# Performance work log

Measured on AMD Instinct MI355X. Metric: run time of the kernel, lower is better.

Reference implementation:

```python
import jax, jax.numpy as jnp
import numpy as np


def _laplacian_kernel(x, z, bandwidth):
    x_sq = jnp.sum(x * x, axis=-1, keepdims=True)          # [N, 1]
    z_sq = jnp.sum(z * z, axis=-1)[None, :]                # [1, M]
    d2 = x_sq + z_sq - 2.0 * jnp.einsum('nd,md->nm', x, z)  # [N, M]
    d = jnp.sqrt(jnp.maximum(d2, 0.0))
    return jnp.exp(-d / bandwidth)


def setup_inputs() -> dict:
    key = jax.random.key(0)
    k1, k2, k3 = jax.random.split(key, 3)
    N, M, D, Y = 8192, 20000, 1024, 256
    batch = jax.random.normal(k1, (N, D), dtype=jnp.float32)
    centers = jax.random.normal(k2, (M, D), dtype=jnp.float32)
    weight = jax.random.normal(k3, (M, Y), dtype=jnp.float32) * 0.02
    return {"batch": batch, "centers": centers, "weight": weight, "bandwidth": 10}


def reference(batch, centers, weight, bandwidth):
    kmat = _laplacian_kernel(batch, centers, float(bandwidth))  # [N, M]
    pred = kmat @ weight                                        # [N, Y]
    return pred
```

## Files before the change

kernel.cpp:

```cpp
#include <hip/hip_runtime.h>
#include <stdint.h>

#define N_ROWS 8192
#define D_DIM  1024
#define M_CENT 20000
#define M_PAD  20224
#define M_TILES 79
#define Y_DIM  256
#define BM 64
#define BN 256
#define MSPLIT 8
#define TILES_PER_SPLIT 10
#define LDSP_STRIDE 264
#define NKT 32
#define PANEL_X (NKT * 512)
#define NKT_M 632
#define PANEL_W (NKT_M * 512)


typedef __attribute__((ext_vector_type(4))) float  f32x4;
typedef __attribute__((ext_vector_type(8))) __bf16 bf16x8;

__device__ __forceinline__ unsigned short f2bf(float f) {
    union { float f; unsigned u; } v; v.f = f;
    unsigned u = v.u;
    u += 0x7FFFu + ((u >> 16) & 1u);
    return (unsigned short)(u >> 16);
}

__global__ void pack_rows_kernel(const float* __restrict__ src,
                                 unsigned short* __restrict__ dst,
                                 float* __restrict__ sq, int nrows_valid) {
    int row = blockIdx.x;
    int t = threadIdx.x;
    int p = row >> 4, m = row & 15;
    float s = 0.f;
    ushort4 o = make_ushort4(0, 0, 0, 0);
    if (row < nrows_valid) {
        float4 v = ((const float4*)(src + (size_t)row * D_DIM))[t];
        s = v.x * v.x + v.y * v.y + v.z * v.z + v.w * v.w;
        o.x = f2bf(v.x); o.y = f2bf(v.y); o.z = f2bf(v.z); o.w = f2bf(v.w);
    }
    size_t obase = (size_t)p * PANEL_X + (size_t)(t >> 3) * 512
                 + (size_t)((t >> 1) & 3) * 128 + m * 8 + (t & 1) * 4;
    *(ushort4*)(dst + obase) = o;
    __shared__ float red[4];
    for (int off = 32; off; off >>= 1) s += __shfl_down(s, off, 64);
    if ((t & 63) == 0) red[t >> 6] = s;
    __syncthreads();
    if (t == 0) sq[row] = red[0] + red[1] + red[2] + red[3];
}

__global__ void pack_wT_kernel(const float* __restrict__ w,
                               unsigned short* __restrict__ wTp) {
    __shared__ float tile[32][33];
    int m0 = blockIdx.x * 32;
    int y0 = blockIdx.y * 32;
    int tx = threadIdx.x & 31;
    int ty = threadIdx.x >> 5;
    #pragma unroll
    for (int i = 0; i < 4; ++i) {
        int mm = m0 + ty + i * 8;
        float v = (mm < M_CENT) ? w[(size_t)mm * Y_DIM + y0 + tx] : 0.f;
        tile[tx][ty + i * 8] = v;
    }
    __syncthreads();
    #pragma unroll
    for (int i = 0; i < 4; ++i) {
        int yl = ty + i * 8;
        int p = (y0 >> 4) + (yl >> 4);
        size_t off = (size_t)p * PANEL_W + (size_t)(m0 >> 5) * 512
                   + (size_t)(tx >> 3) * 128 + (yl & 15) * 8 + (tx & 7);
        wTp[off] = f2bf(tile[yl][tx]);
    }
}

__global__ void __launch_bounds__(256, 2)
fused_kernel(const unsigned short* __restrict__ Xp,
             const unsigned short* __restrict__ Zp,
             const unsigned short* __restrict__ WTp,
             const float* __restrict__ xsq,
             const float* __restrict__ zsq,
             const int* __restrict__ bwp,
             float* __restrict__ out) {
    __shared__ unsigned short lds_p[BM * LDSP_STRIDE];
    __shared__ float lds_xsq[BM];

    const int t    = threadIdx.x;
    const int wave = t >> 6;
    const int lane = t & 63;
    const int quad = lane >> 4;
    const int l16  = lane & 15;
    const int lane8 = lane * 8;

    const int row0 = blockIdx.x * BM;
    int mt = blockIdx.y * TILES_PER_SPLIT;
    int mt_end = mt + TILES_PER_SPLIT;
    if (mt_end > M_TILES) mt_end = M_TILES;

    int bwi = *bwp;
    float bw;
    if (bwi > 0 && bwi < 1000000) bw = (float)bwi;
    else { union { int i; float f; } u; u.i = bwi; bw = u.f; }
    const float inv_bw = 1.0f / bw;

    if (t < BM) lds_xsq[t] = xsq[row0 + t];

    const unsigned short* xp0 = Xp + (size_t)(row0 >> 4) * PANEL_X + lane8;

    const f32x4 vzero = {0.f, 0.f, 0.f, 0.f};
    f32x4 Oacc[16];
    #pragma unroll
    for (int i = 0; i < 16; ++i) Oacc[i] = vzero;

    #pragma unroll 1
    for (; mt < mt_end; ++mt) {
        const int m0 = mt * BN;
        const unsigned short* zp0 = Zp + (size_t)(mt * 16 + wave * 4) * PANEL_X + lane8;

        float zqv[4];
        #pragma unroll
        for (int jt = 0; jt < 4; ++jt)
            zqv[jt] = zsq[m0 + wave * 64 + jt * 16 + l16];

        f32x4 S[16];
        #pragma unroll
        for (int i = 0; i < 16; ++i) S[i] = vzero;

        bf16x8 ae[4], be[4], ao[4], bo[4];
        #pragma unroll
        for (int i = 0; i < 4; ++i) {
            ae[i] = *(const bf16x8*)(xp0 + (size_t)i * PANEL_X);
            be[i] = *(const bf16x8*)(zp0 + (size_t)i * PANEL_X);
        }
        #pragma unroll 1
        for (int kt2 = 0; kt2 < NKT / 2; ++kt2) {
            const unsigned short* xk = xp0 + (size_t)(2 * kt2 + 1) * 512;
            const unsigned short* zk = zp0 + (size_t)(2 * kt2 + 1) * 512;
            #pragma unroll
            for (int i = 0; i < 4; ++i) {
                ao[i] = *(const bf16x8*)(xk + (size_t)i * PANEL_X);
                bo[i] = *(const bf16x8*)(zk + (size_t)i * PANEL_X);
            }
            #pragma unroll
            for (int it = 0; it < 4; ++it)
                #pragma unroll
                for (int jt = 0; jt < 4; ++jt)
                    S[it * 4 + jt] = __builtin_amdgcn_mfma_f32_16x16x32_bf16(
                        ae[it], be[jt], S[it * 4 + jt], 0, 0, 0);
            #pragma unroll
            for (int i = 0; i < 4; ++i) {
                ae[i] = *(const bf16x8*)(xk + 512 + (size_t)i * PANEL_X);
                be[i] = *(const bf16x8*)(zk + 512 + (size_t)i * PANEL_X);
            }
            #pragma unroll
            for (int it = 0; it < 4; ++it)
                #pragma unroll
                for (int jt = 0; jt < 4; ++jt)
                    S[it * 4 + jt] = __builtin_amdgcn_mfma_f32_16x16x32_bf16(
                        ao[it], bo[jt], S[it * 4 + jt], 0, 0, 0);
        }

        __syncthreads();
        #pragma unroll
        for (int it = 0; it < 4; ++it) {
            #pragma unroll
            for (int jt = 0; jt < 4; ++jt) {
                f32x4 s4 = S[it * 4 + jt];
                const int col = wave * 64 + jt * 16 + l16;
                const float zq = zqv[jt];
                #pragma unroll
                for (int r = 0; r < 4; ++r) {
                    const int row = it * 16 + quad * 4 + r;
                    float d2 = lds_xsq[row] + zq - 2.0f * s4[r];
                    d2 = fmaxf(d2, 0.f);
                    float p = __expf(-sqrtf(d2) * inv_bw);
                    lds_p[row * LDSP_STRIDE + col] = f2bf(p);
                }
            }
        }
        __syncthreads();

        #pragma unroll
        for (int ks = 0; ks < 8; ++ks) {
            const int koff = ks * 32 + quad * 8;
            bf16x8 a[4], b[4];
            #pragma unroll
            for (int rt = 0; rt < 4; ++rt)
                a[rt] = *(const bf16x8*)&lds_p[(rt * 16 + l16) * LDSP_STRIDE + koff];
            #pragma unroll
            for (int ct = 0; ct < 4; ++ct)
                b[ct] = *(const bf16x8*)(WTp + (size_t)(wave * 4 + ct) * PANEL_W
                                             + (size_t)(mt * 8 + ks) * 512 + lane8);
            #pragma unroll
            for (int rt = 0; rt < 4; ++rt)
                #pragma unroll
                for (int ct = 0; ct < 4; ++ct)
                    Oacc[rt * 4 + ct] = __builtin_amdgcn_mfma_f32_16x16x32_bf16(
                        a[rt], b[ct], Oacc[rt * 4 + ct], 0, 0, 0);
        }
    }

    #pragma unroll
    for (int rt = 0; rt < 4; ++rt) {
        #pragma unroll
        for (int ct = 0; ct < 4; ++ct) {
            f32x4 v = Oacc[rt * 4 + ct];
            const int y = wave * 64 + ct * 16 + l16;
            #pragma unroll
            for (int r = 0; r < 4; ++r) {
                const int row = row0 + rt * 16 + quad * 4 + r;
                atomicAdd(&out[(size_t)row * Y_DIM + y], v[r]);
            }
        }
    }
}

extern "C" void kernel_launch(void* const* d_in, const int* in_sizes, int n_in,
                              void* d_out, int out_size, void* d_ws, size_t ws_size,
                              hipStream_t stream) {
    const float* X = (const float*)d_in[0];
    const float* Z = (const float*)d_in[1];
    const float* W = (const float*)d_in[2];
    const int*  bw = (const int*)d_in[3];
    float* out = (float*)d_out;

    char* ws = (char*)d_ws;
    size_t off = 0;
    unsigned short* Xp  = (unsigned short*)(ws + off); off += (size_t)N_ROWS * D_DIM * 2;
    unsigned short* Zp  = (unsigned short*)(ws + off); off += (size_t)M_PAD * D_DIM * 2;
    unsigned short* WTp = (unsigned short*)(ws + off); off += (size_t)Y_DIM * M_PAD * 2;
    float* xsq = (float*)(ws + off); off += (size_t)N_ROWS * 4;
    float* zsq = (float*)(ws + off); off += (size_t)M_PAD * 4;

    hipMemsetAsync(d_out, 0, (size_t)out_size * sizeof(float), stream);
    pack_rows_kernel<<<N_ROWS, 256, 0, stream>>>(X, Xp, xsq, N_ROWS);
    pack_rows_kernel<<<M_PAD, 256, 0, stream>>>(Z, Zp, zsq, M_CENT);
    pack_wT_kernel<<<dim3(M_PAD / 32, Y_DIM / 32), 256, 0, stream>>>(W, WTp);
    fused_kernel<<<dim3(N_ROWS / BM, MSPLIT), 256, 0, stream>>>(Xp, Zp, WTp, xsq, zsq, bw, out);
}
```

Baseline: 809.6 us.

## Stage shared X tile in LDS via direct global-to-LDS loads and swizzle P tile

Each wave previously loaded the same X fragments from global memory on its own. Now the block cooperatively loads each k-group of X into an LDS staging buffer with global_load_lds, and all four waves read from it, which cuts redundant global/L2 traffic. The P tile layout moves from a padded stride to an XOR swizzle to avoid LDS bank conflicts, and xsq values are held in registers instead of LDS. This adds two barriers per k-group and more LDS use, which may reduce overlap between loads and MFMA work and affect occupancy.

New measurement: 848.6 us. 1.05x slower.

```diff
diff --git a/kernel.cpp b/kernel.cpp
--- a/kernel.cpp
+++ b/kernel.cpp
@@ -11,8 +11,9 @@
 #define BN 256
 #define MSPLIT 8
 #define TILES_PER_SPLIT 10
-#define LDSP_STRIDE 264
 #define NKT 32
+#define GKT 8
+#define NG  4
 #define PANEL_X (NKT * 512)
 #define NKT_M 632
 #define PANEL_W (NKT_M * 512)
@@ -26,6 +27,12 @@
     unsigned u = v.u;
     u += 0x7FFFu + ((u >> 16) & 1u);
     return (unsigned short)(u >> 16);
+}
+
+__device__ __forceinline__ void gll16(void* lds, const void* g) {
+    __builtin_amdgcn_global_load_lds(
+        (const __attribute__((address_space(1))) void*)g,
+        (__attribute__((address_space(3))) void*)lds, 16, 0, 0);
 }
 
 __global__ void pack_rows_kernel(const float* __restrict__ src,
@@ -83,8 +90,8 @@
              const float* __restrict__ zsq,
              const int* __restrict__ bwp,
              float* __restrict__ out) {
-    __shared__ unsigned short lds_p[BM * LDSP_STRIDE];
-    __shared__ float lds_xsq[BM];
+    __shared__ unsigned short x_stage[BM * 256];
+    __shared__ unsigned short lds_p[BM * BN];
 
     const int t    = threadIdx.x;
     const int wave = t >> 6;
@@ -104,9 +111,16 @@
     else { union { int i; float f; } u; u.i = bwi; bw = u.f; }
     const float inv_bw = 1.0f / bw;
 
-    if (t < BM) lds_xsq[t] = xsq[row0 + t];
-
-    const unsigned short* xp0 = Xp + (size_t)(row0 >> 4) * PANEL_X + lane8;
+    float xsqv[16];
+    #pragma unroll
+    for (int i = 0; i < 16; ++i)
+        xsqv[i] = xsq[row0 + (i >> 2) * 16 + quad * 4 + (i & 3)];
+
+    const int s_it  = t >> 6;
+    const int s_l16 = (t & 63) >> 2;
+    const int s_quad = t & 3;
+    const unsigned short* xsrc = Xp + (size_t)((row0 >> 4) + s_it) * PANEL_X
+                               + s_quad * 128 + s_l16 * 8;
 
     const f32x4 vzero = {0.f, 0.f, 0.f, 0.f};
     f32x4 Oacc[16];
@@ -115,67 +129,89 @@
 
     #pragma unroll 1
     for (; mt < mt_end; ++mt) {
-        const int m0 = mt * BN;
         const unsigned short* zp0 = Zp + (size_t)(mt * 16 + wave * 4) * PANEL_X + lane8;
 
         float zqv[4];
         #pragma unroll
         for (int jt = 0; jt < 4; ++jt)
-            zqv[jt] = zsq[m0 + wave * 64 + jt * 16 + l16];
+            zqv[jt] = zsq[mt * BN + wave * 64 + jt * 16 + l16];
 
         f32x4 S[16];
         #pragma unroll
         for (int i = 0; i < 16; ++i) S[i] = vzero;
 
-        bf16x8 ae[4], be[4], ao[4], bo[4];
-        #pragma unroll
-        for (int i = 0; i < 4; ++i) {
-            ae[i] = *(const bf16x8*)(xp0 + (size_t)i * PANEL_X);
-            be[i] = *(const bf16x8*)(zp0 + (size_t)i * PANEL_X);
-        }
+        bf16x8 ae[4], ao[4], be[4], bo[4];
+        #pragma unroll
+        for (int j = 0; j < 4; ++j)
+            be[j] = *(const bf16x8*)(zp0 + (size_t)j * PANEL_X);
+
         #pragma unroll 1
-        for (int kt2 = 0; kt2 < NKT / 2; ++kt2) {
-            const unsigned short* xk = xp0 + (size_t)(2 * kt2 + 1) * 512;
-            const unsigned short* zk = zp0 + (size_t)(2 * kt2 + 1) * 512;
-            #pragma unroll
-            for (int i = 0; i < 4; ++i) {
-                ao[i] = *(const bf16x8*)(xk + (size_t)i * PANEL_X);
-                bo[i] = *(const bf16x8*)(zk + (size_t)i * PANEL_X);
-            }
-            #pragma unroll
-            for (int it = 0; it < 4; ++it)
-                #pragma unroll
-                for (int jt = 0; jt < 4; ++jt)
-                    S[it * 4 + jt] = __builtin_amdgcn_mfma_f32_16x16x32_bf16(
-                        ae[it], be[jt], S[it * 4 + jt], 0, 0, 0);
-            #pragma unroll
-            for (int i = 0; i < 4; ++i) {
-                ae[i] = *(const bf16x8*)(xk + 512 + (size_t)i * PANEL_X);
-                be[i] = *(const bf16x8*)(zk + 512 + (size_t)i * PANEL_X);
-            }
-            #pragma unroll
-            for (int it = 0; it < 4; ++it)
-                #pragma unroll
-                for (int jt = 0; jt < 4; ++jt)
-                    S[it * 4 + jt] = __builtin_amdgcn_mfma_f32_16x16x32_bf16(
-                        ao[it], bo[jt], S[it * 4 + jt], 0, 0, 0);
-        }
-
-        __syncthreads();
+        for (int g = 0; g < NG; ++g) {
+            __syncthreads();
+            const unsigned short* xg = xsrc + (size_t)(g * GKT) * 512;
+            #pragma unroll
+            for (int i = 0; i < GKT; ++i)
+                gll16(&x_stage[(i * 256 + t) * 8], xg + (size_t)i * 512);
+            __syncthreads();
+            #pragma unroll
+            for (int i = 0; i < 4; ++i)
+                ae[i] = *(const bf16x8*)&x_stage[i * 512 + l16 * 32 + quad * 8];
+
+            #pragma unroll
+            for (int kp = 0; kp < GKT / 2; ++kp) {
+                const int kt = g * GKT + kp * 2;
+                #pragma unroll
+                for (int i = 0; i < 4; ++i)
+                    ao[i] = *(const bf16x8*)&x_stage[(kp * 2 + 1) * 2048
+                                                     + i * 512 + l16 * 32 + quad * 8];
+                {
+                    const unsigned short* zk = zp0 + (size_t)(kt + 1) * 512;
+                    #pragma unroll
+                    for (int j = 0; j < 4; ++j)
+                        bo[j] = *(const bf16x8*)(zk + (size_t)j * PANEL_X);
+                }
+                #pragma unroll
+                for (int it = 0; it < 4; ++it)
+                    #pragma unroll
+                    for (int jt = 0; jt < 4; ++jt)
+                        S[it * 4 + jt] = __builtin_amdgcn_mfma_f32_16x16x32_bf16(
+                            ae[it], be[jt], S[it * 4 + jt], 0, 0, 0);
+                if (kp < GKT / 2 - 1) {
+                    #pragma unroll
+                    for (int i = 0; i < 4; ++i)
+                        ae[i] = *(const bf16x8*)&x_stage[(kp * 2 + 2) * 2048
+                                                         + i * 512 + l16 * 32 + quad * 8];
+                }
+                {
+                    const unsigned short* zk = zp0 + (size_t)(kt + 2) * 512;
+                    #pragma unroll
+                    for (int j = 0; j < 4; ++j)
+                        be[j] = *(const bf16x8*)(zk + (size_t)j * PANEL_X);
+                }
+                #pragma unroll
+                for (int it = 0; it < 4; ++it)
+                    #pragma unroll
+                    for (int jt = 0; jt < 4; ++jt)
+                        S[it * 4 + jt] = __builtin_amdgcn_mfma_f32_16x16x32_bf16(
+                            ao[it], bo[jt], S[it * 4 + jt], 0, 0, 0);
+            }
+        }
+
         #pragma unroll
         for (int it = 0; it < 4; ++it) {
             #pragma unroll
             for (int jt = 0; jt < 4; ++jt) {
                 f32x4 s4 = S[it * 4 + jt];
                 const int col = wave * 64 + jt * 16 + l16;
+                const int ch0 = col >> 3, cl = col & 7;
                 const float zq = zqv[jt];
                 #pragma unroll
                 for (int r = 0; r < 4; ++r) {
                     const int row = it * 16 + quad * 4 + r;
-                    float d2 = lds_xsq[row] + zq - 2.0f * s4[r];
+                    float d2 = xsqv[it * 4 + r] + zq - 2.0f * s4[r];
                     d2 = fmaxf(d2, 0.f);
                     float p = __expf(-sqrtf(d2) * inv_bw);
-                    lds_p[row * LDSP_STRIDE + col] = f2bf(p);
+                    lds_p[row * 256 + ((ch0 ^ (row & 7)) << 3) + cl] = f2bf(p);
                 }
             }
         }
@@ -183,11 +219,13 @@
 
         #pragma unroll
         for (int ks = 0; ks < 8; ++ks) {
-            const int koff = ks * 32 + quad * 8;
             bf16x8 a[4], b[4];
             #pragma unroll
-            for (int rt = 0; rt < 4; ++rt)
-                a[rt] = *(const bf16x8*)&lds_p[(rt * 16 + l16) * LDSP_STRIDE + koff];
+            for (int rt = 0; rt < 4; ++rt) {
+                const int row = rt * 16 + l16;
+                a[rt] = *(const bf16x8*)&lds_p[row * 256
+                          + (((ks * 4 + quad) ^ (l16 & 7)) << 3)];
+            }
             #pragma unroll
             for (int ct = 0; ct < 4; ++ct)
                 b[ct] = *(const bf16x8*)(WTp + (size_t)(wave * 4 + ct) * PANEL_W
```
